# Kernel optimization log

Hardware: AMD Instinct MI355X
Metric: run time of the kernel (lower is better)

The kernel has to match this reference:

```python
import jax, jax.numpy as jnp
import numpy as np

NUM_USER = 1_000_000
NUM_ITEM = 500_000
EMBED_DIM = 64
NUM_EDGES = 2_000_000


def setup_inputs() -> dict:
    key = jax.random.key(0)
    k1, k2, k3, k4 = jax.random.split(key, 4)
    # init_func: uniform_(-0.001, 0.001)
    user_embed = jax.random.uniform(k1, (NUM_USER, EMBED_DIM), dtype=jnp.float32,
                                    minval=-0.001, maxval=0.001)
    item_embed = jax.random.uniform(k2, (NUM_ITEM, EMBED_DIM), dtype=jnp.float32,
                                    minval=-0.001, maxval=0.001)
    edge_src = jax.random.randint(k3, (NUM_EDGES,), 0, NUM_USER, dtype=jnp.int64
                                  if jax.config.jax_enable_x64 else jnp.int32)
    edge_dst = jax.random.randint(k4, (NUM_EDGES,), 0, NUM_ITEM, dtype=jnp.int64
                                  if jax.config.jax_enable_x64 else jnp.int32)
    return {"user_embed": user_embed, "item_embed": item_embed,
            "edge_src": edge_src, "edge_dst": edge_dst}


def reference(user_embed, item_embed, edge_src, edge_dst):
    """Faithful to NGCF.forward: every conv layer is fed `vecs` (the original
    embeddings), and HeteroGraphConv over the single user->item 'checkin'
    relation (SAGEConv mean, weight=False, bias=False) outputs only 'item'
    features; intermediate leaky_relu results are overwritten. Net effect:
    one unweighted mean-aggregation of user embeddings onto item nodes."""
    # gather user features along edges: [E, D]
    gathered = user_embed[edge_src]
    sums = jax.ops.segment_sum(gathered, edge_dst, num_segments=NUM_ITEM)
    counts = jax.ops.segment_sum(jnp.ones((edge_dst.shape[0],), dtype=user_embed.dtype),
                                 edge_dst, num_segments=NUM_ITEM)
    # mean aggregation; items with no in-edges get zeros (DGL behavior)
    item_out = sums / jnp.maximum(counts, 1.0)[:, None]
    return item_out
```

## Files before the change

kernel.cpp:

```cpp
#include <hip/hip_runtime.h>

#define NUM_ITEM 500000
#define EMBED_DIM 64
#define PAD 16


__global__ __launch_bounds__(256) void scatter_pad(
    const int* __restrict__ edge_src, const int* __restrict__ edge_dst,
    int num_edges, int* __restrict__ cnt, int* __restrict__ pad,
    int* __restrict__ ovf, int* __restrict__ ovf_n, int ovf_cap)
{
    int e = blockIdx.x * 256 + threadIdx.x;
    if (e >= num_edges) return;
    int d = edge_dst[e];
    int s = edge_src[e];
    int slot = atomicAdd(&cnt[d], 1);
    if (slot < PAD) {
        pad[(size_t)d * PAD + slot] = s;
    } else {
        int o = atomicAdd(ovf_n, 1);
        if (o < ovf_cap) { ovf[2 * o] = d; ovf[2 * o + 1] = s; }
    }
}

__global__ __launch_bounds__(256) void gather_pad(
    const float* __restrict__ user_embed, const int* __restrict__ pad,
    const int* __restrict__ cnt, float* __restrict__ out, int n_items)
{
    int item = blockIdx.x * 4 + (threadIdx.x >> 6);
    int lane = threadIdx.x & 63;
    if (item >= n_items) return;

    const int* p = pad + (size_t)item * PAD;
    int c = cnt[item];
    int4 i0 = *(const int4*)p;
    int4 i1 = *(const int4*)(p + 4);
    int sidx[8] = {i0.x, i0.y, i0.z, i0.w, i1.x, i1.y, i1.z, i1.w};

    float sum = 0.f;
#pragma unroll
    for (int e = 0; e < 8; ++e) {
        int s = (e < c) ? sidx[e] : 0;
        float v = user_embed[(size_t)s * EMBED_DIM + lane];
        sum += (e < c) ? v : 0.f;
    }
    int cc = (c < PAD) ? c : PAD;
    for (int e = 8; e < cc; ++e) {
        int s = p[e];
        sum += user_embed[(size_t)s * EMBED_DIM + lane];
    }
    float denom = (c > 0) ? (float)c : 1.0f;
    out[(size_t)item * EMBED_DIM + lane] = sum / denom;
}

__global__ __launch_bounds__(256) void fixup_overflow(
    const float* __restrict__ user_embed, const int* __restrict__ ovf,
    const int* __restrict__ ovf_n, const int* __restrict__ cnt,
    float* __restrict__ out, int ovf_cap)
{
    int n = *ovf_n;
    if (n > ovf_cap) n = ovf_cap;
    int wave = blockIdx.x * 4 + (threadIdx.x >> 6);
    int lane = threadIdx.x & 63;
    int nwaves = gridDim.x * 4;
    for (int i = wave; i < n; i += nwaves) {
        int d = ovf[2 * i];
        int s = ovf[2 * i + 1];
        float v = user_embed[(size_t)s * EMBED_DIM + lane] / (float)cnt[d];
        atomicAdd(&out[(size_t)d * EMBED_DIM + lane], v);
    }
}


__global__ __launch_bounds__(256) void histogram_dst(
    const int* __restrict__ edge_dst, int num_edges, int* __restrict__ counts)
{
    int e = blockIdx.x * blockDim.x + threadIdx.x;
    if (e >= num_edges) return;
    atomicAdd(&counts[edge_dst[e]], 1);
}

__global__ __launch_bounds__(256) void block_sums(
    const int* __restrict__ counts, int n, int* __restrict__ partials)
{
    __shared__ int red[256];
    int i = blockIdx.x * 256 + threadIdx.x;
    red[threadIdx.x] = (i < n) ? counts[i] : 0;
    __syncthreads();
    for (int s = 128; s > 0; s >>= 1) {
        if (threadIdx.x < (unsigned)s) red[threadIdx.x] += red[threadIdx.x + s];
        __syncthreads();
    }
    if (threadIdx.x == 0) partials[blockIdx.x] = red[0];
}

__global__ __launch_bounds__(256) void scan_partials(int* __restrict__ partials, int nb)
{
    __shared__ int tmp[256];
    __shared__ int carry_s;
    if (threadIdx.x == 0) carry_s = 0;
    __syncthreads();
    for (int base = 0; base < nb; base += 256) {
        int i = base + threadIdx.x;
        int v = (i < nb) ? partials[i] : 0;
        tmp[threadIdx.x] = v;
        __syncthreads();
        for (int off = 1; off < 256; off <<= 1) {
            int t = (threadIdx.x >= (unsigned)off) ? tmp[threadIdx.x - off] : 0;
            __syncthreads();
            tmp[threadIdx.x] += t;
            __syncthreads();
        }
        int incl = tmp[threadIdx.x];
        int c = carry_s;
        if (i < nb) partials[i] = incl - v + c;
        __syncthreads();
        if (threadIdx.x == 255) carry_s = c + tmp[255];
        __syncthreads();
    }
}

__global__ __launch_bounds__(256) void make_offsets(
    const int* __restrict__ counts, const int* __restrict__ partials, int n,
    int* __restrict__ offsets, int* __restrict__ cursor)
{
    __shared__ int tmp[256];
    int i = blockIdx.x * 256 + threadIdx.x;
    int v = (i < n) ? counts[i] : 0;
    tmp[threadIdx.x] = v;
    __syncthreads();
    for (int off = 1; off < 256; off <<= 1) {
        int t = (threadIdx.x >= (unsigned)off) ? tmp[threadIdx.x - off] : 0;
        __syncthreads();
        tmp[threadIdx.x] += t;
        __syncthreads();
    }
    int excl = tmp[threadIdx.x] - v + partials[blockIdx.x];
    if (i < n) { offsets[i] = excl; cursor[i] = excl; }
}

__global__ __launch_bounds__(256) void scatter_csr(
    const int* __restrict__ edge_src, const int* __restrict__ edge_dst,
    int num_edges, int* __restrict__ cursor, int* __restrict__ csr_src)
{
    int e = blockIdx.x * blockDim.x + threadIdx.x;
    if (e >= num_edges) return;
    int d = edge_dst[e];
    int pos = atomicAdd(&cursor[d], 1);
    csr_src[pos] = edge_src[e];
}

__global__ __launch_bounds__(256) void gather_mean(
    const float* __restrict__ user_embed, const int* __restrict__ csr_src,
    const int* __restrict__ offsets, const int* __restrict__ counts,
    float* __restrict__ out, int n_items)
{
    int item = blockIdx.x * 4 + (threadIdx.x >> 6);
    int lane = threadIdx.x & 63;
    if (item >= n_items) return;
    int off = offsets[item];
    int cnt = counts[item];
    float sum = 0.f;
    for (int e = 0; e < cnt; ++e) {
        int s = csr_src[off + e];
        sum += user_embed[(size_t)s * EMBED_DIM + lane];
    }
    float denom = (cnt > 0) ? (float)cnt : 1.0f;
    out[(size_t)item * EMBED_DIM + lane] = sum / denom;
}


__global__ __launch_bounds__(256) void scatter_mean_accum(
    const float* __restrict__ user_embed,
    const int* __restrict__ edge_src,
    const int* __restrict__ edge_dst,
    float* __restrict__ sums, float* __restrict__ counts, int num_edges)
{
    const int edge = blockIdx.x * (blockDim.x >> 6) + (threadIdx.x >> 6);
    const int lane = threadIdx.x & 63;
    if (edge >= num_edges) return;
    const int s = edge_src[edge];
    const int d = edge_dst[edge];
    atomicAdd(&sums[(size_t)d * EMBED_DIM + lane],
              user_embed[(size_t)s * EMBED_DIM + lane]);
    if (lane == 0) atomicAdd(&counts[d], 1.0f);
}

__global__ __launch_bounds__(256) void divide_by_count(
    float* __restrict__ out, const float* __restrict__ counts, int n)
{
    const int idx = blockIdx.x * blockDim.x + threadIdx.x;
    if (idx >= n) return;
    out[idx] = out[idx] / fmaxf(counts[idx >> 6], 1.0f);
}


extern "C" void kernel_launch(void* const* d_in, const int* in_sizes, int n_in,
                              void* d_out, int out_size, void* d_ws, size_t ws_size,
                              hipStream_t stream)
{
    const float* user_embed = (const float*)d_in[0];
    const int* edge_src = (const int*)d_in[2];
    const int* edge_dst = (const int*)d_in[3];
    const int num_edges = in_sizes[2];
    float* out = (float*)d_out;

    const int eb = (num_edges + 255) / 256;

    const size_t hdr_b = 64;
    const size_t cnt_b = (size_t)NUM_ITEM * 4;
    const size_t pad_b = (size_t)NUM_ITEM * PAD * 4;
    const size_t fixed = hdr_b + cnt_b + pad_b;
    long long cap_ll = ((long long)ws_size - (long long)fixed) / 8;
    if (cap_ll > num_edges) cap_ll = num_edges;
    const int min_cap = (num_edges < 4096) ? num_edges : 4096;

    if (cap_ll >= min_cap) {
        char* ws = (char*)d_ws;
        int* ovf_n = (int*)ws;
        int* cnt   = (int*)(ws + hdr_b);
        int* pad   = (int*)(ws + hdr_b + cnt_b);
        int* ovf   = (int*)(ws + fixed);
        const int ovf_cap = (int)cap_ll;

        hipMemsetAsync(d_ws, 0, hdr_b + cnt_b, stream);
        scatter_pad<<<eb, 256, 0, stream>>>(edge_src, edge_dst, num_edges,
                                            cnt, pad, ovf, ovf_n, ovf_cap);
        gather_pad<<<(NUM_ITEM + 3) / 4, 256, 0, stream>>>(
            user_embed, pad, cnt, out, NUM_ITEM);
        fixup_overflow<<<64, 256, 0, stream>>>(user_embed, ovf, ovf_n, cnt,
                                               out, ovf_cap);
        return;
    }

    const int NB = (NUM_ITEM + 255) / 256;
    const size_t counts_b   = (size_t)NUM_ITEM * 4;
    const size_t offsets_b  = (size_t)NUM_ITEM * 4;
    const size_t cursor_b   = (size_t)NUM_ITEM * 4;
    const size_t partials_b = 2048 * 4;
    const size_t csr_b      = (size_t)num_edges * 4;
    const size_t needed = counts_b + offsets_b + cursor_b + partials_b + csr_b;

    if (ws_size >= needed) {
        char* ws = (char*)d_ws;
        int* counts   = (int*)ws;                         ws += counts_b;
        int* offsets  = (int*)ws;                         ws += offsets_b;
        int* cursor   = (int*)ws;                         ws += cursor_b;
        int* partials = (int*)ws;                         ws += partials_b;
        int* csr_src  = (int*)ws;

        hipMemsetAsync(counts, 0, counts_b, stream);
        histogram_dst<<<eb, 256, 0, stream>>>(edge_dst, num_edges, counts);
        block_sums<<<NB, 256, 0, stream>>>(counts, NUM_ITEM, partials);
        scan_partials<<<1, 256, 0, stream>>>(partials, NB);
        make_offsets<<<NB, 256, 0, stream>>>(counts, partials, NUM_ITEM, offsets, cursor);
        scatter_csr<<<eb, 256, 0, stream>>>(edge_src, edge_dst, num_edges, cursor, csr_src);
        gather_mean<<<(NUM_ITEM + 3) / 4, 256, 0, stream>>>(
            user_embed, csr_src, offsets, counts, out, NUM_ITEM);
    } else {
        float* counts = (float*)d_ws;
        hipMemsetAsync(d_out, 0, (size_t)NUM_ITEM * EMBED_DIM * sizeof(float), stream);
        hipMemsetAsync(d_ws, 0, (size_t)NUM_ITEM * sizeof(float), stream);
        const int blocks = (num_edges + 3) / 4;
        scatter_mean_accum<<<blocks, 256, 0, stream>>>(
            user_embed, edge_src, edge_dst, out, counts, num_edges);
        const int n = NUM_ITEM * EMBED_DIM;
        divide_by_count<<<(n + 255) / 256, 256, 0, stream>>>(out, counts, n);
    }
}
```

Measured before the change: 674.1 us.

## Shrink pad to 8 slots and gather with float4 lanes plus shuffle reduction

Halves the per-item padded slot array to 8 entries, so items with more than 8 in-edges go to the overflow list, which is processed by more fixup blocks. The gather kernel now splits each wave into 4 groups of 16 lanes; each group loads two rows as float4 and the groups are combined with xor shuffles, with a nontemporal vector store of the result. This targets less pad memory traffic and more memory-level parallelism per wave. In exchange, overflow atomics grow for high-degree items (mean degree is 4, so a small tail) and the minimum overflow capacity rises.

```diff
diff --git a/kernel.cpp b/kernel.cpp
--- a/kernel.cpp
+++ b/kernel.cpp
@@ -2,7 +2,9 @@
 
 #define NUM_ITEM 500000
 #define EMBED_DIM 64
-#define PAD 16
+#define PAD 8
+
+typedef float f4_native __attribute__((ext_vector_type(4)));
 
 
 __global__ __launch_bounds__(256) void scatter_pad(
@@ -30,27 +32,50 @@
     int item = blockIdx.x * 4 + (threadIdx.x >> 6);
     int lane = threadIdx.x & 63;
     if (item >= n_items) return;
+    int g = lane >> 4;
+    int q = lane & 15;
 
     const int* p = pad + (size_t)item * PAD;
     int c = cnt[item];
     int4 i0 = *(const int4*)p;
     int4 i1 = *(const int4*)(p + 4);
-    int sidx[8] = {i0.x, i0.y, i0.z, i0.w, i1.x, i1.y, i1.z, i1.w};
-
-    float sum = 0.f;
-#pragma unroll
-    for (int e = 0; e < 8; ++e) {
-        int s = (e < c) ? sidx[e] : 0;
-        float v = user_embed[(size_t)s * EMBED_DIM + lane];
-        sum += (e < c) ? v : 0.f;
-    }
-    int cc = (c < PAD) ? c : PAD;
-    for (int e = 8; e < cc; ++e) {
-        int s = p[e];
-        sum += user_embed[(size_t)s * EMBED_DIM + lane];
-    }
-    float denom = (c > 0) ? (float)c : 1.0f;
-    out[(size_t)item * EMBED_DIM + lane] = sum / denom;
+
+    int s0 = (g == 0) ? i0.x : (g == 1) ? i0.y : (g == 2) ? i0.z : i0.w;
+    int s1 = (g == 0) ? i1.x : (g == 1) ? i1.y : (g == 2) ? i1.z : i1.w;
+    bool v0 = (g < c);
+    bool v1 = (4 + g < c);
+    s0 = v0 ? s0 : 0;
+    s1 = v1 ? s1 : 0;
+
+    const float* r0 = user_embed + ((size_t)(unsigned)s0 << 6) + (q << 2);
+    const float* r1 = user_embed + ((size_t)(unsigned)s1 << 6) + (q << 2);
+    float4 a = *(const float4*)r0;
+    float4 b = *(const float4*)r1;
+
+    float4 acc;
+    acc.x = (v0 ? a.x : 0.f) + (v1 ? b.x : 0.f);
+    acc.y = (v0 ? a.y : 0.f) + (v1 ? b.y : 0.f);
+    acc.z = (v0 ? a.z : 0.f) + (v1 ? b.z : 0.f);
+    acc.w = (v0 ? a.w : 0.f) + (v1 ? b.w : 0.f);
+
+    acc.x += __shfl_xor(acc.x, 16, 64);
+    acc.y += __shfl_xor(acc.y, 16, 64);
+    acc.z += __shfl_xor(acc.z, 16, 64);
+    acc.w += __shfl_xor(acc.w, 16, 64);
+    acc.x += __shfl_xor(acc.x, 32, 64);
+    acc.y += __shfl_xor(acc.y, 32, 64);
+    acc.z += __shfl_xor(acc.z, 32, 64);
+    acc.w += __shfl_xor(acc.w, 32, 64);
+
+    float inv = 1.0f / ((c > 0) ? (float)c : 1.0f);
+    acc.x *= inv; acc.y *= inv; acc.z *= inv; acc.w *= inv;
+
+    if (g == 0) {
+        f4_native nv;
+        nv.x = acc.x; nv.y = acc.y; nv.z = acc.z; nv.w = acc.w;
+        __builtin_nontemporal_store(
+            nv, (f4_native*)(out + ((size_t)item << 6) + (q << 2)));
+    }
 }
 
 __global__ __launch_bounds__(256) void fixup_overflow(
@@ -213,7 +238,7 @@
     const size_t fixed = hdr_b + cnt_b + pad_b;
     long long cap_ll = ((long long)ws_size - (long long)fixed) / 8;
     if (cap_ll > num_edges) cap_ll = num_edges;
-    const int min_cap = (num_edges < 4096) ? num_edges : 4096;
+    const int min_cap = (num_edges < 65536) ? num_edges : 65536;
 
     if (cap_ll >= min_cap) {
         char* ws = (char*)d_ws;
@@ -223,13 +248,13 @@
         int* ovf   = (int*)(ws + fixed);
         const int ovf_cap = (int)cap_ll;
 
-        hipMemsetAsync(d_ws, 0, hdr_b + cnt_b, stream);
+        (void)hipMemsetAsync(d_ws, 0, hdr_b + cnt_b, stream);
         scatter_pad<<<eb, 256, 0, stream>>>(edge_src, edge_dst, num_edges,
                                             cnt, pad, ovf, ovf_n, ovf_cap);
         gather_pad<<<(NUM_ITEM + 3) / 4, 256, 0, stream>>>(
             user_embed, pad, cnt, out, NUM_ITEM);
-        fixup_overflow<<<64, 256, 0, stream>>>(user_embed, ovf, ovf_n, cnt,
-                                               out, ovf_cap);
+        fixup_overflow<<<512, 256, 0, stream>>>(user_embed, ovf, ovf_n, cnt,
+                                                out, ovf_cap);
         return;
     }
 
@@ -249,7 +274,7 @@
         int* partials = (int*)ws;                         ws += partials_b;
         int* csr_src  = (int*)ws;
 
-        hipMemsetAsync(counts, 0, counts_b, stream);
+        (void)hipMemsetAsync(counts, 0, counts_b, stream);
         histogram_dst<<<eb, 256, 0, stream>>>(edge_dst, num_edges, counts);
         block_sums<<<NB, 256, 0, stream>>>(counts, NUM_ITEM, partials);
         scan_partials<<<1, 256, 0, stream>>>(partials, NB);
@@ -259,8 +284,8 @@
             user_embed, csr_src, offsets, counts, out, NUM_ITEM);
     } else {
         float* counts = (float*)d_ws;
-        hipMemsetAsync(d_out, 0, (size_t)NUM_ITEM * EMBED_DIM * sizeof(float), stream);
-        hipMemsetAsync(d_ws, 0, (size_t)NUM_ITEM * sizeof(float), stream);
+        (void)hipMemsetAsync(d_out, 0, (size_t)NUM_ITEM * EMBED_DIM * sizeof(float), stream);
+        (void)hipMemsetAsync(d_ws, 0, (size_t)NUM_ITEM * sizeof(float), stream);
         const int blocks = (num_edges + 3) / 4;
         scatter_mean_accum<<<blocks, 256, 0, stream>>>(
             user_embed, edge_src, edge_dst, out, counts, num_edges);
```

Result: slower. 750.5 us (+11.3%).
